# Kernel optimization log

Measured on AMD Instinct MI355X. Metric: run time of the kernel, lower is better.

Reference implementation:

```python
import jax, jax.numpy as jnp
import numpy as np

B, S, E = 1, 8192, 1024

def setup_inputs() -> dict:
    key = jax.random.key(0)
    ks = jax.random.split(key, 7)
    scale = 1.0 / np.sqrt(E)
    q = jax.random.normal(ks[0], (B, S, E), dtype=jnp.float32)
    Wq = jax.random.uniform(ks[1], (E, E), jnp.float32, -scale, scale)
    bq = jax.random.uniform(ks[2], (E,), jnp.float32, -scale, scale)
    Wk = jax.random.uniform(ks[3], (E, E), jnp.float32, -scale, scale)
    bk = jax.random.uniform(ks[4], (E,), jnp.float32, -scale, scale)
    Wv = jax.random.uniform(ks[5], (E, E), jnp.float32, -scale, scale)
    bv = jax.random.uniform(ks[6], (E,), jnp.float32, -scale, scale)
    return {"q": q, "Wq": Wq, "bq": bq, "Wk": Wk, "bk": bk, "Wv": Wv, "bv": bv}

def reference(q, Wq, bq, Wk, bk, Wv, bv):
    # k and v default to q in the original module
    Q = jnp.einsum('bse,fe->bsf', q, Wq) + bq          # [B,S,E]
    K = jnp.einsum('bse,fe->bsf', q, Wk) + bk          # [B,S,E]
    V = jnp.einsum('bse,fe->bsf', q, Wv) + bv          # [B,S,E]
    weights = jax.nn.softmax(K, axis=1)                # softmax over sequence dim
    # sum over seq -> [B,E], then sum over E keepdim -> [B,1] (faithful to source)
    weighted_context = jnp.sum(weights * V, axis=1).sum(axis=1, keepdims=True)
    Y = jax.nn.sigmoid(Q) * weighted_context           # broadcast (valid since B==1)
    return Y
```

## Files before the change

### kernel.cpp

```cpp
#include <hip/hip_runtime.h>
#include <hip/hip_bf16.h>
#include <stdint.h>

typedef __bf16 bf16_t;
typedef __bf16 bf16x8 __attribute__((ext_vector_type(8)));
typedef float f32x4 __attribute__((ext_vector_type(4)));

#define E_DIM 1024
#define S_DIM 8192

__device__ __forceinline__ void gload_lds16(const void* g, void* l) {
  using gptr_t = const __attribute__((address_space(1))) void*;
  using lptr_t = __attribute__((address_space(3))) void*;
  gptr_t gp = (gptr_t)(uintptr_t)g;
  lptr_t lp = (lptr_t)(uint32_t)(uintptr_t)l;
  __builtin_amdgcn_global_load_lds(gp, lp, 16, 0, 0);
}

__device__ __forceinline__ void cvt8(const float* __restrict__ src,
                                     bf16_t* __restrict__ dst, int i) {
  const float4* s = reinterpret_cast<const float4*>(src) + (size_t)i * 2;
  float4 a = s[0], b = s[1];
  bf16x8 o;
  o[0] = (bf16_t)a.x; o[1] = (bf16_t)a.y; o[2] = (bf16_t)a.z; o[3] = (bf16_t)a.w;
  o[4] = (bf16_t)b.x; o[5] = (bf16_t)b.y; o[6] = (bf16_t)b.z; o[7] = (bf16_t)b.w;
  *reinterpret_cast<bf16x8*>(dst + (size_t)i * 8) = o;
}

__global__ __launch_bounds__(256) void cvt_all(const float* __restrict__ q,
                                               const float* __restrict__ Wk,
                                               const float* __restrict__ Wv,
                                               const float* __restrict__ Wq,
                                               bf16_t* __restrict__ qb,
                                               bf16_t* __restrict__ Wb) {
  const int b = blockIdx.x;
  const int t = threadIdx.x;
  if (b < 4096) {
    cvt8(q, qb, b * 256 + t);
  } else if (b < 4608) {
    cvt8(Wk, Wb, (b - 4096) * 256 + t);
  } else if (b < 5120) {
    cvt8(Wv, Wb + 1048576, (b - 4608) * 256 + t);
  } else {
    cvt8(Wq, Wb + 2097152, (b - 5120) * 256 + t);
  }
}

__global__ __launch_bounds__(256, 2) void gemm_kv(const bf16_t* __restrict__ A,
                                                  const bf16_t* __restrict__ Wk,
                                                  const bf16_t* __restrict__ Wv,
                                                  const float* __restrict__ bk,
                                                  const float* __restrict__ bv,
                                                  float* __restrict__ pden,
                                                  float* __restrict__ pnum) {
  __shared__ bf16_t lA[128 * 32];
  __shared__ bf16_t lK[128 * 32];
  __shared__ bf16_t lV[128 * 32];
  __shared__ float sden[2][128];
  __shared__ float snum[2][128];

  const int tid = threadIdx.x;
  const int wv = tid >> 6;
  const int lane = tid & 63;
  const int m0 = blockIdx.y * 128;
  const int n0 = blockIdx.x * 128;
  const int wr = wv >> 1;
  const int wc = wv & 1;

  f32x4 accK[4][4], accV[4][4];
#pragma unroll
  for (int i = 0; i < 4; ++i)
#pragma unroll
    for (int j = 0; j < 4; ++j) {
      accK[i][j] = (f32x4){0.f, 0.f, 0.f, 0.f};
      accV[i][j] = (f32x4){0.f, 0.f, 0.f, 0.f};
    }

  const int srow = wv * 16 + (lane >> 2);
  const int skk = (lane & 3) * 8;
  const bf16_t* gA0 = A + (size_t)(m0 + srow) * E_DIM + skk;
  const bf16_t* gA1 = gA0 + (size_t)64 * E_DIM;
  const bf16_t* gK0 = Wk + (size_t)(n0 + srow) * E_DIM + skk;
  const bf16_t* gK1 = gK0 + (size_t)64 * E_DIM;
  const bf16_t* gV0 = Wv + (size_t)(n0 + srow) * E_DIM + skk;
  const bf16_t* gV1 = gV0 + (size_t)64 * E_DIM;
  bf16_t* lA0 = &lA[wv * 512];
  bf16_t* lA1 = &lA[(wv + 4) * 512];
  bf16_t* lK0 = &lK[wv * 512];
  bf16_t* lK1 = &lK[(wv + 4) * 512];
  bf16_t* lV0 = &lV[wv * 512];
  bf16_t* lV1 = &lV[(wv + 4) * 512];

  const int frow = lane & 15;
  const int fk = (lane >> 4) * 8;

  for (int k0 = 0; k0 < E_DIM; k0 += 32) {
    gload_lds16(gA0 + k0, lA0);
    gload_lds16(gA1 + k0, lA1);
    gload_lds16(gK0 + k0, lK0);
    gload_lds16(gK1 + k0, lK1);
    gload_lds16(gV0 + k0, lV0);
    gload_lds16(gV1 + k0, lV1);
    __syncthreads();

    bf16x8 af[4], kf[4], vf[4];
#pragma unroll
    for (int m = 0; m < 4; ++m)
      af[m] = *reinterpret_cast<const bf16x8*>(&lA[(wr * 64 + m * 16 + frow) * 32 + fk]);
#pragma unroll
    for (int n = 0; n < 4; ++n) {
      kf[n] = *reinterpret_cast<const bf16x8*>(&lK[(wc * 64 + n * 16 + frow) * 32 + fk]);
      vf[n] = *reinterpret_cast<const bf16x8*>(&lV[(wc * 64 + n * 16 + frow) * 32 + fk]);
    }
#pragma unroll
    for (int m = 0; m < 4; ++m)
#pragma unroll
      for (int n = 0; n < 4; ++n) {
        accK[m][n] = __builtin_amdgcn_mfma_f32_16x16x32_bf16(af[m], kf[n], accK[m][n], 0, 0, 0);
        accV[m][n] = __builtin_amdgcn_mfma_f32_16x16x32_bf16(af[m], vf[n], accV[m][n], 0, 0, 0);
      }
    __syncthreads();
  }

  const int ccol = lane & 15;
#pragma unroll
  for (int n = 0; n < 4; ++n) {
    const int col = n0 + wc * 64 + n * 16 + ccol;
    const float bkc = bk[col];
    const float bvc = bv[col];
    float dp = 0.f, np = 0.f;
#pragma unroll
    for (int m = 0; m < 4; ++m)
#pragma unroll
      for (int r = 0; r < 4; ++r) {
        float e = __expf(accK[m][n][r] + bkc);
        dp += e;
        np += e * (accV[m][n][r] + bvc);
      }
    dp += __shfl_xor(dp, 16); dp += __shfl_xor(dp, 32);
    np += __shfl_xor(np, 16); np += __shfl_xor(np, 32);
    if (lane < 16) {
      sden[wr][wc * 64 + n * 16 + lane] = dp;
      snum[wr][wc * 64 + n * 16 + lane] = np;
    }
  }
  __syncthreads();
  if (tid < 128) {
    float d = sden[0][tid] + sden[1][tid];
    float nm = snum[0][tid] + snum[1][tid];
    pden[(size_t)blockIdx.y * 1024 + n0 + tid] = d;
    pnum[(size_t)blockIdx.y * 1024 + n0 + tid] = nm;
  }
}

__global__ __launch_bounds__(1024) void finalize(const float* __restrict__ pden,
                                                 const float* __restrict__ pnum,
                                                 float* __restrict__ cval) {
  const int t = threadIdx.x;
  float d = 0.f, nm = 0.f;
  for (int b = 0; b < 64; ++b) {
    d += pden[b * 1024 + t];
    nm += pnum[b * 1024 + t];
  }
  float val = nm / d;
  __shared__ float red[1024];
  red[t] = val;
  __syncthreads();
  for (int s = 512; s > 0; s >>= 1) {
    if (t < s) red[t] += red[t + s];
    __syncthreads();
  }
  if (t == 0) cval[0] = red[0];
}

__global__ __launch_bounds__(256) void gemm_q(const bf16_t* __restrict__ A,
                                              const bf16_t* __restrict__ B,
                                              float* __restrict__ C,
                                              const float* __restrict__ bias,
                                              const float* __restrict__ cptr) {
  __shared__ bf16_t lA[128 * 32];
  __shared__ bf16_t lB[128 * 32];

  const int tid = threadIdx.x;
  const int wv = tid >> 6;
  const int lane = tid & 63;
  const int m0 = blockIdx.y * 128;
  const int n0 = blockIdx.x * 128;
  const int wr = wv >> 1;
  const int wc = wv & 1;

  f32x4 acc[4][4];
#pragma unroll
  for (int i = 0; i < 4; ++i)
#pragma unroll
    for (int j = 0; j < 4; ++j) acc[i][j] = (f32x4){0.f, 0.f, 0.f, 0.f};

  const int srow = wv * 16 + (lane >> 2);
  const int skk = (lane & 3) * 8;
  const bf16_t* gA0 = A + (size_t)(m0 + srow) * E_DIM + skk;
  const bf16_t* gA1 = gA0 + (size_t)64 * E_DIM;
  const bf16_t* gB0 = B + (size_t)(n0 + srow) * E_DIM + skk;
  const bf16_t* gB1 = gB0 + (size_t)64 * E_DIM;
  bf16_t* lA0 = &lA[wv * 512];
  bf16_t* lA1 = &lA[(wv + 4) * 512];
  bf16_t* lB0 = &lB[wv * 512];
  bf16_t* lB1 = &lB[(wv + 4) * 512];

  const int frow = lane & 15;
  const int fk = (lane >> 4) * 8;

  for (int k0 = 0; k0 < E_DIM; k0 += 32) {
    gload_lds16(gA0 + k0, lA0);
    gload_lds16(gA1 + k0, lA1);
    gload_lds16(gB0 + k0, lB0);
    gload_lds16(gB1 + k0, lB1);
    __syncthreads();

    bf16x8 af[4], bfr[4];
#pragma unroll
    for (int m = 0; m < 4; ++m)
      af[m] = *reinterpret_cast<const bf16x8*>(&lA[(wr * 64 + m * 16 + frow) * 32 + fk]);
#pragma unroll
    for (int n = 0; n < 4; ++n)
      bfr[n] = *reinterpret_cast<const bf16x8*>(&lB[(wc * 64 + n * 16 + frow) * 32 + fk]);
#pragma unroll
    for (int m = 0; m < 4; ++m)
#pragma unroll
      for (int n = 0; n < 4; ++n)
        acc[m][n] = __builtin_amdgcn_mfma_f32_16x16x32_bf16(af[m], bfr[n], acc[m][n], 0, 0, 0);
    __syncthreads();
  }

  const float cv = cptr[0];
  const int crow = (lane >> 4) * 4;
  const int ccol = lane & 15;
#pragma unroll
  for (int n = 0; n < 4; ++n) {
    const int col = n0 + wc * 64 + n * 16 + ccol;
    const float bs = bias[col];
#pragma unroll
    for (int m = 0; m < 4; ++m) {
      const int row = m0 + wr * 64 + m * 16 + crow;
#pragma unroll
      for (int r = 0; r < 4; ++r) {
        float v = acc[m][n][r] + bs;
        v = cv / (1.f + __expf(-v));
        C[(size_t)(row + r) * 1024 + col] = v;
      }
    }
  }
}

extern "C" void kernel_launch(void* const* d_in, const int* in_sizes, int n_in,
                              void* d_out, int out_size, void* d_ws, size_t ws_size,
                              hipStream_t stream) {
  const float* q = (const float*)d_in[0];
  const float* Wq = (const float*)d_in[1];
  const float* bq = (const float*)d_in[2];
  const float* Wk = (const float*)d_in[3];
  const float* bk = (const float*)d_in[4];
  const float* Wv = (const float*)d_in[5];
  const float* bv = (const float*)d_in[6];
  float* out = (float*)d_out;

  char* ws = (char*)d_ws;
  bf16_t* qb = (bf16_t*)ws;
  bf16_t* Wb = (bf16_t*)(ws + (size_t)16 * 1024 * 1024);
  float* pden = (float*)(ws + (size_t)24 * 1024 * 1024);
  float* pnum = pden + 64 * 1024;
  float* cval = pnum + 64 * 1024;

  cvt_all<<<5632, 256, 0, stream>>>(q, Wk, Wv, Wq, qb, Wb);
  gemm_kv<<<dim3(8, 64), 256, 0, stream>>>(qb, Wb, Wb + 1048576, bk, bv, pden, pnum);
  finalize<<<1, 1024, 0, stream>>>(pden, pnum, cval);
  gemm_q<<<dim3(8, 64), 256, 0, stream>>>(qb, Wb + 2097152, out, bq, cval);
}
```

Before: 91.04 us.

## Interleave Wk/Wv rows and use 8-wave double-buffered swizzled GEMM kernels

Converts Wk and Wv into one interleaved [2048x1024] bf16 matrix so a single GEMM computes K and V columns side by side; the V value is fetched from the neighbouring lane with a shuffle. Both GEMMs move to 512-thread blocks with 256-wide tiles, a K-step of 64, double-buffered LDS staging, an XOR swizzle against bank conflicts, staged prefetch with explicit waitcnt and barriers, setprio around the MFMA bursts, and block-index swizzling for L2 reuse. The aim is more MFMA throughput and less LDS and global-load stall. In exchange it uses much more LDS and registers per block (one block per CU), and the hand-written vmcnt counts must stay in step with the number of issued loads.

```diff
diff --git a/kernel.cpp b/kernel.cpp
--- a/kernel.cpp
+++ b/kernel.cpp
@@ -6,8 +6,7 @@
 typedef __bf16 bf16x8 __attribute__((ext_vector_type(8)));
 typedef float f32x4 __attribute__((ext_vector_type(4)));
 
-#define E_DIM 1024
-#define S_DIM 8192
+#define NKT 16
 
 __device__ __forceinline__ void gload_lds16(const void* g, void* l) {
   using gptr_t = const __attribute__((address_space(1))) void*;
@@ -17,140 +16,196 @@
   __builtin_amdgcn_global_load_lds(gp, lp, 16, 0, 0);
 }
 
-__device__ __forceinline__ void cvt8(const float* __restrict__ src,
-                                     bf16_t* __restrict__ dst, int i) {
-  const float4* s = reinterpret_cast<const float4*>(src) + (size_t)i * 2;
+__device__ __forceinline__ bf16x8 cvt8v(const float* __restrict__ src, int i8) {
+  const float4* s = reinterpret_cast<const float4*>(src) + (size_t)i8 * 2;
   float4 a = s[0], b = s[1];
   bf16x8 o;
   o[0] = (bf16_t)a.x; o[1] = (bf16_t)a.y; o[2] = (bf16_t)a.z; o[3] = (bf16_t)a.w;
   o[4] = (bf16_t)b.x; o[5] = (bf16_t)b.y; o[6] = (bf16_t)b.z; o[7] = (bf16_t)b.w;
-  *reinterpret_cast<bf16x8*>(dst + (size_t)i * 8) = o;
+  return o;
 }
 
 __global__ __launch_bounds__(256) void cvt_all(const float* __restrict__ q,
                                                const float* __restrict__ Wk,
                                                const float* __restrict__ Wv,
                                                const float* __restrict__ Wq,
+                                               const float* __restrict__ bk,
+                                               const float* __restrict__ bv,
                                                bf16_t* __restrict__ qb,
-                                               bf16_t* __restrict__ Wb) {
+                                               bf16_t* __restrict__ Wkv,
+                                               bf16_t* __restrict__ Wqb,
+                                               float* __restrict__ bkv) {
   const int b = blockIdx.x;
   const int t = threadIdx.x;
   if (b < 4096) {
-    cvt8(q, qb, b * 256 + t);
+    int i = b * 256 + t;
+    *reinterpret_cast<bf16x8*>(qb + (size_t)i * 8) = cvt8v(q, i);
   } else if (b < 4608) {
-    cvt8(Wk, Wb, (b - 4096) * 256 + t);
+    int i = (b - 4096) * 256 + t;
+    int j = i >> 7, c8 = i & 127;
+    *reinterpret_cast<bf16x8*>(Wkv + (size_t)j * 2048 + c8 * 8) = cvt8v(Wk, i);
   } else if (b < 5120) {
-    cvt8(Wv, Wb + 1048576, (b - 4608) * 256 + t);
+    int i = (b - 4608) * 256 + t;
+    int j = i >> 7, c8 = i & 127;
+    *reinterpret_cast<bf16x8*>(Wkv + (size_t)j * 2048 + 1024 + c8 * 8) = cvt8v(Wv, i);
+  } else if (b < 5632) {
+    int i = (b - 5120) * 256 + t;
+    *reinterpret_cast<bf16x8*>(Wqb + (size_t)i * 8) = cvt8v(Wq, i);
   } else {
-    cvt8(Wq, Wb + 2097152, (b - 5120) * 256 + t);
-  }
-}
-
-__global__ __launch_bounds__(256, 2) void gemm_kv(const bf16_t* __restrict__ A,
-                                                  const bf16_t* __restrict__ Wk,
-                                                  const bf16_t* __restrict__ Wv,
-                                                  const float* __restrict__ bk,
-                                                  const float* __restrict__ bv,
-                                                  float* __restrict__ pden,
-                                                  float* __restrict__ pnum) {
-  __shared__ bf16_t lA[128 * 32];
-  __shared__ bf16_t lK[128 * 32];
-  __shared__ bf16_t lV[128 * 32];
-  __shared__ float sden[2][128];
-  __shared__ float snum[2][128];
+#pragma unroll
+    for (int u = 0; u < 4; ++u) {
+      int j = t * 4 + u;
+      bkv[2 * j] = bk[j];
+      bkv[2 * j + 1] = bv[j];
+    }
+  }
+}
+
+__global__ __launch_bounds__(512, 1) void gemm_kv8(const bf16_t* __restrict__ A,
+                                                   const bf16_t* __restrict__ Bkv,
+                                                   const float* __restrict__ bkv,
+                                                   float* __restrict__ pden,
+                                                   float* __restrict__ pnum) {
+  __shared__ bf16_t lA[2 * 256 * 64];
+  __shared__ bf16_t lB[2 * 256 * 64];
+  __shared__ float sD[2][128];
+  __shared__ float sN[2][128];
 
   const int tid = threadIdx.x;
-  const int wv = tid >> 6;
-  const int lane = tid & 63;
-  const int m0 = blockIdx.y * 128;
-  const int n0 = blockIdx.x * 128;
-  const int wr = wv >> 1;
-  const int wc = wv & 1;
-
-  f32x4 accK[4][4], accV[4][4];
-#pragma unroll
-  for (int i = 0; i < 4; ++i)
-#pragma unroll
-    for (int j = 0; j < 4; ++j) {
-      accK[i][j] = (f32x4){0.f, 0.f, 0.f, 0.f};
-      accV[i][j] = (f32x4){0.f, 0.f, 0.f, 0.f};
-    }
-
-  const int srow = wv * 16 + (lane >> 2);
-  const int skk = (lane & 3) * 8;
-  const bf16_t* gA0 = A + (size_t)(m0 + srow) * E_DIM + skk;
-  const bf16_t* gA1 = gA0 + (size_t)64 * E_DIM;
-  const bf16_t* gK0 = Wk + (size_t)(n0 + srow) * E_DIM + skk;
-  const bf16_t* gK1 = gK0 + (size_t)64 * E_DIM;
-  const bf16_t* gV0 = Wv + (size_t)(n0 + srow) * E_DIM + skk;
-  const bf16_t* gV1 = gV0 + (size_t)64 * E_DIM;
-  bf16_t* lA0 = &lA[wv * 512];
-  bf16_t* lA1 = &lA[(wv + 4) * 512];
-  bf16_t* lK0 = &lK[wv * 512];
-  bf16_t* lK1 = &lK[(wv + 4) * 512];
-  bf16_t* lV0 = &lV[wv * 512];
-  bf16_t* lV1 = &lV[(wv + 4) * 512];
-
-  const int frow = lane & 15;
-  const int fk = (lane >> 4) * 8;
-
-  for (int k0 = 0; k0 < E_DIM; k0 += 32) {
-    gload_lds16(gA0 + k0, lA0);
-    gload_lds16(gA1 + k0, lA1);
-    gload_lds16(gK0 + k0, lK0);
-    gload_lds16(gK1 + k0, lK1);
-    gload_lds16(gV0 + k0, lV0);
-    gload_lds16(gV1 + k0, lV1);
-    __syncthreads();
-
-    bf16x8 af[4], kf[4], vf[4];
+  const int w = tid >> 6, l = tid & 63;
+  const int wr = w >> 2, wc = w & 3;
+  const int swz = (blockIdx.x & 7) * 32 + (blockIdx.x >> 3);
+  const int bx = swz & 7, by = swz >> 3;
+  const int m0 = by * 256, n0 = bx * 256;
+
+  const int rl3 = l >> 3;
+  const int scol = ((l & 7) ^ rl3) * 8;
+  const int fr = l & 15, fg = l >> 4, sw = l & 7;
+
+  const bf16_t* Ab = A + (size_t)(m0 + w * 8 + rl3) * 1024 + scol;
+  const bf16_t* Bb = Bkv + (size_t)(n0 + w * 8 + rl3) * 1024 + scol;
+
+  f32x4 acc[8][4];
+#pragma unroll
+  for (int m = 0; m < 8; ++m)
+#pragma unroll
+    for (int n = 0; n < 4; ++n) acc[m][n] = (f32x4){0.f, 0.f, 0.f, 0.f};
+
+#define STAGE_A(kt, h, r, slot)                                              \
+  gload_lds16(Ab + (size_t)((h) * 128 + (r) * 64) * 1024 + (kt) * 64,        \
+              &lA[(slot) * 16384 + ((h) * 128 + (r) * 64 + w * 8) * 64])
+#define STAGE_B(kt, h, r, slot)                                              \
+  gload_lds16(Bb + (size_t)((h) * 128 + (r) * 64) * 1024 + (kt) * 64,        \
+              &lB[(slot) * 16384 + ((h) * 128 + (r) * 64 + w * 8) * 64])
+#define RD_A(mm, ks) \
+  (*reinterpret_cast<const bf16x8*>(&lA[aBase + ((mm) * 16 + fr) * 64 + ((((ks) * 4) + fg) ^ sw) * 8]))
+#define RD_B(nn, ks) \
+  (*reinterpret_cast<const bf16x8*>(&lB[bBase + ((nn) * 16 + fr) * 64 + ((((ks) * 4) + fg) ^ sw) * 8]))
+
+  STAGE_A(0, 0, 0, 0); STAGE_A(0, 0, 1, 0); STAGE_A(0, 1, 0, 0); STAGE_A(0, 1, 1, 0);
+  STAGE_B(0, 0, 0, 0); STAGE_B(0, 0, 1, 0); STAGE_B(0, 1, 0, 0); STAGE_B(0, 1, 1, 0);
+
+#pragma unroll 1
+  for (int T = 0; T < NKT; ++T) {
+    const int slot = T & 1, ns = slot ^ 1;
+    const bool pf = (T + 1) < NKT;
+    if (pf) { STAGE_A(T + 1, 0, 0, ns); STAGE_A(T + 1, 0, 1, ns); }
+    if (pf) asm volatile("s_waitcnt vmcnt(2)" ::: "memory");
+    else    asm volatile("s_waitcnt vmcnt(0)" ::: "memory");
+    __builtin_amdgcn_s_barrier();
+    __builtin_amdgcn_sched_barrier(0);
+
+    const int aBase = slot * 16384 + wr * 8192;
+    const int bBase = slot * 16384 + wc * 4096;
+    bf16x8 af[4], bfv[4];
+#pragma unroll
+    for (int n = 0; n < 4; ++n) bfv[n] = RD_B(n, 0);
+#pragma unroll
+    for (int m = 0; m < 4; ++m) af[m] = RD_A(m, 0);
+    if (pf) { STAGE_A(T + 1, 1, 0, ns); STAGE_A(T + 1, 1, 1, ns); }
+    __builtin_amdgcn_s_setprio(1);
 #pragma unroll
     for (int m = 0; m < 4; ++m)
-      af[m] = *reinterpret_cast<const bf16x8*>(&lA[(wr * 64 + m * 16 + frow) * 32 + fk]);
+#pragma unroll
+      for (int n = 0; n < 4; ++n)
+        acc[m][n] = __builtin_amdgcn_mfma_f32_16x16x32_bf16(af[m], bfv[n], acc[m][n], 0, 0, 0);
+    __builtin_amdgcn_s_setprio(0);
+    __builtin_amdgcn_s_barrier();
+    __builtin_amdgcn_sched_barrier(0);
+#pragma unroll
+    for (int m = 0; m < 4; ++m) af[m] = RD_A(m + 4, 0);
+    if (pf) { STAGE_B(T + 1, 0, 0, ns); STAGE_B(T + 1, 0, 1, ns); }
+    __builtin_amdgcn_s_setprio(1);
+#pragma unroll
+    for (int m = 0; m < 4; ++m)
+#pragma unroll
+      for (int n = 0; n < 4; ++n)
+        acc[m + 4][n] = __builtin_amdgcn_mfma_f32_16x16x32_bf16(af[m], bfv[n], acc[m + 4][n], 0, 0, 0);
+    __builtin_amdgcn_s_setprio(0);
+    __builtin_amdgcn_s_barrier();
+    __builtin_amdgcn_sched_barrier(0);
+#pragma unroll
+    for (int n = 0; n < 4; ++n) bfv[n] = RD_B(n, 1);
+#pragma unroll
+    for (int m = 0; m < 4; ++m) af[m] = RD_A(m, 1);
+    if (pf) { STAGE_B(T + 1, 1, 0, ns); STAGE_B(T + 1, 1, 1, ns); }
+    __builtin_amdgcn_s_setprio(1);
+#pragma unroll
+    for (int m = 0; m < 4; ++m)
+#pragma unroll
+      for (int n = 0; n < 4; ++n)
+        acc[m][n] = __builtin_amdgcn_mfma_f32_16x16x32_bf16(af[m], bfv[n], acc[m][n], 0, 0, 0);
+    __builtin_amdgcn_s_setprio(0);
+    __builtin_amdgcn_s_barrier();
+    __builtin_amdgcn_sched_barrier(0);
+#pragma unroll
+    for (int m = 0; m < 4; ++m) af[m] = RD_A(m + 4, 1);
+    __builtin_amdgcn_s_setprio(1);
+#pragma unroll
+    for (int m = 0; m < 4; ++m)
+#pragma unroll
+      for (int n = 0; n < 4; ++n)
+        acc[m + 4][n] = __builtin_amdgcn_mfma_f32_16x16x32_bf16(af[m], bfv[n], acc[m + 4][n], 0, 0, 0);
+    __builtin_amdgcn_s_setprio(0);
+    __builtin_amdgcn_s_barrier();
+    __builtin_amdgcn_sched_barrier(0);
+  }
+
+  float dpn[4] = {0.f, 0.f, 0.f, 0.f};
+  float npn[4] = {0.f, 0.f, 0.f, 0.f};
+#pragma unroll
+  for (int n = 0; n < 4; ++n) {
+    const int col = n0 + wc * 64 + n * 16 + fr;
+    const float bc = bkv[col];
+#pragma unroll
+    for (int m = 0; m < 8; ++m)
+#pragma unroll
+      for (int r = 0; r < 4; ++r) {
+        float x = acc[m][n][r] + bc;
+        float xp = __shfl_xor(x, 1);
+        float e = __expf(x);
+        dpn[n] += e;
+        npn[n] += e * xp;
+      }
+    dpn[n] += __shfl_xor(dpn[n], 16); dpn[n] += __shfl_xor(dpn[n], 32);
+    npn[n] += __shfl_xor(npn[n], 16); npn[n] += __shfl_xor(npn[n], 32);
+  }
+  if (l < 16 && (l & 1) == 0) {
 #pragma unroll
     for (int n = 0; n < 4; ++n) {
-      kf[n] = *reinterpret_cast<const bf16x8*>(&lK[(wc * 64 + n * 16 + frow) * 32 + fk]);
-      vf[n] = *reinterpret_cast<const bf16x8*>(&lV[(wc * 64 + n * 16 + frow) * 32 + fk]);
-    }
-#pragma unroll
-    for (int m = 0; m < 4; ++m)
-#pragma unroll
-      for (int n = 0; n < 4; ++n) {
-        accK[m][n] = __builtin_amdgcn_mfma_f32_16x16x32_bf16(af[m], kf[n], accK[m][n], 0, 0, 0);
-        accV[m][n] = __builtin_amdgcn_mfma_f32_16x16x32_bf16(af[m], vf[n], accV[m][n], 0, 0, 0);
-      }
-    __syncthreads();
-  }
-
-  const int ccol = lane & 15;
-#pragma unroll
-  for (int n = 0; n < 4; ++n) {
-    const int col = n0 + wc * 64 + n * 16 + ccol;
-    const float bkc = bk[col];
-    const float bvc = bv[col];
-    float dp = 0.f, np = 0.f;
-#pragma unroll
-    for (int m = 0; m < 4; ++m)
-#pragma unroll
-      for (int r = 0; r < 4; ++r) {
-        float e = __expf(accK[m][n][r] + bkc);
-        dp += e;
-        np += e * (accV[m][n][r] + bvc);
-      }
-    dp += __shfl_xor(dp, 16); dp += __shfl_xor(dp, 32);
-    np += __shfl_xor(np, 16); np += __shfl_xor(np, 32);
-    if (lane < 16) {
-      sden[wr][wc * 64 + n * 16 + lane] = dp;
-      snum[wr][wc * 64 + n * 16 + lane] = np;
+      sD[wr][wc * 32 + n * 8 + (l >> 1)] = dpn[n];
+      sN[wr][wc * 32 + n * 8 + (l >> 1)] = npn[n];
     }
   }
   __syncthreads();
   if (tid < 128) {
-    float d = sden[0][tid] + sden[1][tid];
-    float nm = snum[0][tid] + snum[1][tid];
-    pden[(size_t)blockIdx.y * 1024 + n0 + tid] = d;
-    pnum[(size_t)blockIdx.y * 1024 + n0 + tid] = nm;
-  }
+    pden[(size_t)by * 1024 + bx * 128 + tid] = sD[0][tid] + sD[1][tid];
+    pnum[(size_t)by * 1024 + bx * 128 + tid] = sN[0][tid] + sN[1][tid];
+  }
+#undef STAGE_A
+#undef STAGE_B
+#undef RD_A
+#undef RD_B
 }
 
 __global__ __launch_bounds__(1024) void finalize(const float* __restrict__ pden,
@@ -158,7 +213,7 @@
                                                  float* __restrict__ cval) {
   const int t = threadIdx.x;
   float d = 0.f, nm = 0.f;
-  for (int b = 0; b < 64; ++b) {
+  for (int b = 0; b < 32; ++b) {
     d += pden[b * 1024 + t];
     nm += pnum[b * 1024 + t];
   }
@@ -173,74 +228,118 @@
   if (t == 0) cval[0] = red[0];
 }
 
-__global__ __launch_bounds__(256) void gemm_q(const bf16_t* __restrict__ A,
-                                              const bf16_t* __restrict__ B,
-                                              float* __restrict__ C,
-                                              const float* __restrict__ bias,
-                                              const float* __restrict__ cptr) {
-  __shared__ bf16_t lA[128 * 32];
-  __shared__ bf16_t lB[128 * 32];
+__global__ __launch_bounds__(512, 1) void gemm_q8(const bf16_t* __restrict__ A,
+                                                  const bf16_t* __restrict__ Bq,
+                                                  const float* __restrict__ bias,
+                                                  const float* __restrict__ cptr,
+                                                  float* __restrict__ C) {
+  __shared__ bf16_t lA[2 * 256 * 64];
+  __shared__ bf16_t lB[2 * 128 * 64];
 
   const int tid = threadIdx.x;
-  const int wv = tid >> 6;
-  const int lane = tid & 63;
-  const int m0 = blockIdx.y * 128;
-  const int n0 = blockIdx.x * 128;
-  const int wr = wv >> 1;
-  const int wc = wv & 1;
+  const int w = tid >> 6, l = tid & 63;
+  const int wr = w >> 1, wc = w & 1;
+  const int swz = (blockIdx.x & 7) * 32 + (blockIdx.x >> 3);
+  const int bx = swz & 7, by = swz >> 3;
+  const int m0 = by * 256, n0 = bx * 128;
+
+  const int rl3 = l >> 3;
+  const int scol = ((l & 7) ^ rl3) * 8;
+  const int fr = l & 15, fg = l >> 4, sw = l & 7;
+
+  const bf16_t* Ab = A + (size_t)(m0 + w * 8 + rl3) * 1024 + scol;
+  const bf16_t* Bb = Bq + (size_t)(n0 + w * 8 + rl3) * 1024 + scol;
 
   f32x4 acc[4][4];
 #pragma unroll
-  for (int i = 0; i < 4; ++i)
-#pragma unroll
-    for (int j = 0; j < 4; ++j) acc[i][j] = (f32x4){0.f, 0.f, 0.f, 0.f};
-
-  const int srow = wv * 16 + (lane >> 2);
-  const int skk = (lane & 3) * 8;
-  const bf16_t* gA0 = A + (size_t)(m0 + srow) * E_DIM + skk;
-  const bf16_t* gA1 = gA0 + (size_t)64 * E_DIM;
-  const bf16_t* gB0 = B + (size_t)(n0 + srow) * E_DIM + skk;
-  const bf16_t* gB1 = gB0 + (size_t)64 * E_DIM;
-  bf16_t* lA0 = &lA[wv * 512];
-  bf16_t* lA1 = &lA[(wv + 4) * 512];
-  bf16_t* lB0 = &lB[wv * 512];
-  bf16_t* lB1 = &lB[(wv + 4) * 512];
-
-  const int frow = lane & 15;
-  const int fk = (lane >> 4) * 8;
-
-  for (int k0 = 0; k0 < E_DIM; k0 += 32) {
-    gload_lds16(gA0 + k0, lA0);
-    gload_lds16(gA1 + k0, lA1);
-    gload_lds16(gB0 + k0, lB0);
-    gload_lds16(gB1 + k0, lB1);
-    __syncthreads();
-
-    bf16x8 af[4], bfr[4];
-#pragma unroll
-    for (int m = 0; m < 4; ++m)
-      af[m] = *reinterpret_cast<const bf16x8*>(&lA[(wr * 64 + m * 16 + frow) * 32 + fk]);
-#pragma unroll
-    for (int n = 0; n < 4; ++n)
-      bfr[n] = *reinterpret_cast<const bf16x8*>(&lB[(wc * 64 + n * 16 + frow) * 32 + fk]);
-#pragma unroll
-    for (int m = 0; m < 4; ++m)
-#pragma unroll
-      for (int n = 0; n < 4; ++n)
-        acc[m][n] = __builtin_amdgcn_mfma_f32_16x16x32_bf16(af[m], bfr[n], acc[m][n], 0, 0, 0);
-    __syncthreads();
+  for (int m = 0; m < 4; ++m)
+#pragma unroll
+    for (int n = 0; n < 4; ++n) acc[m][n] = (f32x4){0.f, 0.f, 0.f, 0.f};
+
+#define STAGE_A(kt, h, r, slot)                                              \
+  gload_lds16(Ab + (size_t)((h) * 128 + (r) * 64) * 1024 + (kt) * 64,        \
+              &lA[(slot) * 16384 + ((h) * 128 + (r) * 64 + w * 8) * 64])
+#define STAGE_B(kt, h, slot)                                                 \
+  gload_lds16(Bb + (size_t)((h) * 64) * 1024 + (kt) * 64,                    \
+              &lB[(slot) * 8192 + ((h) * 64 + w * 8) * 64])
+#define RD_A(mm, ks) \
+  (*reinterpret_cast<const bf16x8*>(&lA[aBase + ((mm) * 16 + fr) * 64 + ((((ks) * 4) + fg) ^ sw) * 8]))
+#define RD_B(nn, ks) \
+  (*reinterpret_cast<const bf16x8*>(&lB[bBase + ((nn) * 16 + fr) * 64 + ((((ks) * 4) + fg) ^ sw) * 8]))
+
+  STAGE_A(0, 0, 0, 0); STAGE_A(0, 0, 1, 0); STAGE_A(0, 1, 0, 0); STAGE_A(0, 1, 1, 0);
+  STAGE_B(0, 0, 0); STAGE_B(0, 1, 0);
+
+#pragma unroll 1
+  for (int T = 0; T < NKT; ++T) {
+    const int slot = T & 1, ns = slot ^ 1;
+    const bool pf = (T + 1) < NKT;
+    if (pf) { STAGE_A(T + 1, 0, 0, ns); STAGE_A(T + 1, 0, 1, ns); }
+    if (pf) asm volatile("s_waitcnt vmcnt(2)" ::: "memory");
+    else    asm volatile("s_waitcnt vmcnt(0)" ::: "memory");
+    __builtin_amdgcn_s_barrier();
+    __builtin_amdgcn_sched_barrier(0);
+
+    const int aBase = slot * 16384 + wr * 4096;
+    const int bBase = slot * 8192 + wc * 4096;
+    bf16x8 af[2], bfv[4];
+#pragma unroll
+    for (int n = 0; n < 4; ++n) bfv[n] = RD_B(n, 0);
+    af[0] = RD_A(0, 0); af[1] = RD_A(1, 0);
+    if (pf) { STAGE_A(T + 1, 1, 0, ns); STAGE_A(T + 1, 1, 1, ns); }
+    __builtin_amdgcn_s_setprio(1);
+#pragma unroll
+    for (int m = 0; m < 2; ++m)
+#pragma unroll
+      for (int n = 0; n < 4; ++n)
+        acc[m][n] = __builtin_amdgcn_mfma_f32_16x16x32_bf16(af[m], bfv[n], acc[m][n], 0, 0, 0);
+    __builtin_amdgcn_s_setprio(0);
+    __builtin_amdgcn_s_barrier();
+    __builtin_amdgcn_sched_barrier(0);
+    af[0] = RD_A(2, 0); af[1] = RD_A(3, 0);
+    if (pf) STAGE_B(T + 1, 0, ns);
+    __builtin_amdgcn_s_setprio(1);
+#pragma unroll
+    for (int m = 0; m < 2; ++m)
+#pragma unroll
+      for (int n = 0; n < 4; ++n)
+        acc[m + 2][n] = __builtin_amdgcn_mfma_f32_16x16x32_bf16(af[m], bfv[n], acc[m + 2][n], 0, 0, 0);
+    __builtin_amdgcn_s_setprio(0);
+    __builtin_amdgcn_s_barrier();
+    __builtin_amdgcn_sched_barrier(0);
+#pragma unroll
+    for (int n = 0; n < 4; ++n) bfv[n] = RD_B(n, 1);
+    af[0] = RD_A(0, 1); af[1] = RD_A(1, 1);
+    if (pf) STAGE_B(T + 1, 1, ns);
+    __builtin_amdgcn_s_setprio(1);
+#pragma unroll
+    for (int m = 0; m < 2; ++m)
+#pragma unroll
+      for (int n = 0; n < 4; ++n)
+        acc[m][n] = __builtin_amdgcn_mfma_f32_16x16x32_bf16(af[m], bfv[n], acc[m][n], 0, 0, 0);
+    __builtin_amdgcn_s_setprio(0);
+    __builtin_amdgcn_s_barrier();
+    __builtin_amdgcn_sched_barrier(0);
+    af[0] = RD_A(2, 1); af[1] = RD_A(3, 1);
+    __builtin_amdgcn_s_setprio(1);
+#pragma unroll
+    for (int m = 0; m < 2; ++m)
+#pragma unroll
+      for (int n = 0; n < 4; ++n)
+        acc[m + 2][n] = __builtin_amdgcn_mfma_f32_16x16x32_bf16(af[m], bfv[n], acc[m + 2][n], 0, 0, 0);
+    __builtin_amdgcn_s_setprio(0);
+    __builtin_amdgcn_s_barrier();
+    __builtin_amdgcn_sched_barrier(0);
   }
 
   const float cv = cptr[0];
-  const int crow = (lane >> 4) * 4;
-  const int ccol = lane & 15;
 #pragma unroll
   for (int n = 0; n < 4; ++n) {
-    const int col = n0 + wc * 64 + n * 16 + ccol;
+    const int col = n0 + wc * 64 + n * 16 + fr;
     const float bs = bias[col];
 #pragma unroll
     for (int m = 0; m < 4; ++m) {
-      const int row = m0 + wr * 64 + m * 16 + crow;
+      const int row = m0 + wr * 64 + m * 16 + fg * 4;
 #pragma unroll
       for (int r = 0; r < 4; ++r) {
         float v = acc[m][n][r] + bs;
@@ -249,6 +348,10 @@
       }
     }
   }
+#undef STAGE_A
+#undef STAGE_B
+#undef RD_A
+#undef RD_B
 }
 
 extern "C" void kernel_launch(void* const* d_in, const int* in_sizes, int n_in,
@@ -265,13 +368,15 @@
 
   char* ws = (char*)d_ws;
   bf16_t* qb = (bf16_t*)ws;
-  bf16_t* Wb = (bf16_t*)(ws + (size_t)16 * 1024 * 1024);
-  float* pden = (float*)(ws + (size_t)24 * 1024 * 1024);
-  float* pnum = pden + 64 * 1024;
-  float* cval = pnum + 64 * 1024;
-
-  cvt_all<<<5632, 256, 0, stream>>>(q, Wk, Wv, Wq, qb, Wb);
-  gemm_kv<<<dim3(8, 64), 256, 0, stream>>>(qb, Wb, Wb + 1048576, bk, bv, pden, pnum);
+  bf16_t* Wkv = (bf16_t*)(ws + (size_t)16 * 1024 * 1024);
+  bf16_t* Wqb = (bf16_t*)(ws + (size_t)20 * 1024 * 1024);
+  float* bkv = (float*)(ws + (size_t)22 * 1024 * 1024);
+  float* pden = (float*)(ws + (size_t)23 * 1024 * 1024);
+  float* pnum = (float*)(ws + (size_t)23 * 1024 * 1024 + 131072);
+  float* cval = (float*)(ws + (size_t)23 * 1024 * 1024 + 262144);
+
+  cvt_all<<<5633, 256, 0, stream>>>(q, Wk, Wv, Wq, bk, bv, qb, Wkv, Wqb, bkv);
+  gemm_kv8<<<256, 512, 0, stream>>>(qb, Wkv, bkv, pden, pnum);
   finalize<<<1, 1024, 0, stream>>>(pden, pnum, cval);
-  gemm_q<<<dim3(8, 64), 256, 0, stream>>>(qb, Wb + 2097152, out, bq, cval);
-}
+  gemm_q8<<<256, 512, 0, stream>>>(qb, Wqb, bq, cval, out);
+}
```

New measurement: 77.84 us. 1.17x faster.
